# Kernel optimization log

Measured on AMD Instinct MI355X. Metric: run time of the kernel, lower is better.

Reference implementation:

```python
import jax, jax.numpy as jnp
import numpy as np

NUM_AGENTS = 256
STATE_DIM = 12 * NUM_AGENTS
CONTROL_DIM = 4 * NUM_AGENTS
MASS = 0.5
HIDDEN = 100
BATCH = 8192


def lambertw(x):
    # Principal branch for x >= 0 via Halley iterations (jit/vjp friendly).
    w = jnp.log1p(x)
    for _ in range(30):
        ew = jnp.exp(w)
        f = w * ew - x
        denom = ew * (w + 1.0) - (w + 2.0) * f / (2.0 * (w + 1.0))
        w = w - f / denom
    return w


def setup_inputs() -> dict:
    key = jax.random.key(0)
    ks = jax.random.split(key, 8)
    scale1 = 1.0 / np.sqrt(STATE_DIM + 1)
    scale2 = 1.0 / np.sqrt(HIDDEN)
    return {
        "z": jax.random.normal(ks[0], (BATCH, STATE_DIM), dtype=jnp.float32),
        "t": jax.random.uniform(ks[1], (BATCH, 1), dtype=jnp.float32),
        "W1": jax.random.normal(ks[2], (STATE_DIM + 1, HIDDEN), dtype=jnp.float32) * scale1,
        "b1": jnp.zeros((HIDDEN,), dtype=jnp.float32),
        "W2": jax.random.normal(ks[3], (HIDDEN, HIDDEN), dtype=jnp.float32) * scale2,
        "b2": jnp.zeros((HIDDEN,), dtype=jnp.float32),
        "W3": jax.random.normal(ks[4], (HIDDEN, STATE_DIM), dtype=jnp.float32) * scale2,
        "b3": jnp.zeros((STATE_DIM,), dtype=jnp.float32),
    }


def reference(z, t, W1, b1, W2, b2, W3, b3):
    # p_net: MLP on (t, z) producing cost parameters p (B, STATE_DIM)
    x = jnp.concatenate([t, z], axis=-1)
    h = jnp.tanh(x @ W1 + b1)
    h = jnp.tanh(h @ W2 + b2)
    p = h @ W3 + b3

    B = p.shape[0]
    pr = p.reshape(B, NUM_AGENTS, 12)
    # Linear cost vector c over controls: agent components (x,y,z adjoints)/m, psi, theta, phi.
    c = jnp.stack(
        [(pr[..., 6] + pr[..., 7] + pr[..., 8]) / MASS, pr[..., 9], pr[..., 10], pr[..., 11]],
        axis=-1,
    ).reshape(B, CONTROL_DIM)

    # Closed-form solution of min_u c^T u + exp(alpha * ||u||^2), alpha = 0.5/N:
    # u* = -k c with 2*alpha*k*exp(alpha*k^2*s) = 1, s = ||c||^2
    # => k = sqrt(W(s/(2*alpha)) / (2*alpha*s))
    alpha = 0.5 / NUM_AGENTS
    s = jnp.sum(c * c, axis=-1)  # (B,)
    w = lambertw(s / (2.0 * alpha))
    safe_s = jnp.where(s > 0, s, 1.0)
    k = jnp.sqrt(w / (2.0 * alpha * safe_s))
    k = jnp.where(s > 0, k, 0.0)
    ustar = -k[:, None] * c  # (B, CONTROL_DIM)
    return ustar
```

## Files before the change

### kernel.cpp

```cpp
#include <hip/hip_runtime.h>

#define DEV __device__ __forceinline__

typedef __bf16 bf16x8 __attribute__((ext_vector_type(8)));
typedef float f32x4 __attribute__((ext_vector_type(4)));
typedef short s16x8 __attribute__((ext_vector_type(8)));
typedef unsigned short u16x8 __attribute__((ext_vector_type(8)));

constexpr int B_ = 8192;
constexpr int S_ = 3072;
constexpr int H_ = 100;
constexpr int NP_ = 128;
constexpr int C_ = 1024;
constexpr int KS_ = 64;
constexpr int NSPLIT_ = 4;
constexpr int KSP_ = S_ / NSPLIT_;
constexpr int NIT_ = KSP_ / KS_;

constexpr size_t OFF_W1b = 0;
constexpr size_t OFF_W2b = OFF_W1b + (size_t)NP_ * S_ * 2;
constexpr size_t OFF_W3c = OFF_W2b + (size_t)NP_ * NP_ * 2;
constexpr size_t OFF_b3c = OFF_W3c + (size_t)C_ * NP_ * 2;
constexpr size_t OFF_part = OFF_b3c + (size_t)C_ * 4;

DEV unsigned short f2bf(float f) {
  union { float f; unsigned u; } x; x.f = f;
  return (unsigned short)((x.u + 0x7FFFu + ((x.u >> 16) & 1u)) >> 16);
}

DEV float lambertw0(float x) {
  float w = log1pf(x);
#pragma unroll
  for (int i = 0; i < 10; ++i) {
    float ew = expf(w);
    float f = fmaf(w, ew, -x);
    float wp1 = w + 1.0f;
    float den = ew * wp1 - (w + 2.0f) * f / (2.0f * wp1);
    w = w - f / den;
  }
  return w;
}

DEV void gload16(const void* g, void* l) {
  __builtin_amdgcn_global_load_lds((const __attribute__((address_space(1))) unsigned int*)g,
                                   (__attribute__((address_space(3))) unsigned int*)l, 16, 0, 0);
}

__global__ void k0_prep(const float* __restrict__ W1, const float* __restrict__ W2,
                        const float* __restrict__ W3, const float* __restrict__ b3,
                        unsigned char* __restrict__ ws) {
  int idx = blockIdx.x * 256 + threadIdx.x;
  constexpr int R1 = NP_ * S_;
  constexpr int R2 = R1 + NP_ * NP_;
  constexpr int R3 = R2 + C_ * NP_;
  constexpr int R4 = R3 + C_;
  if (idx < R1) {
    int n = idx / S_, k = idx - n * S_;
    float v = (n < H_) ? W1[(size_t)(k + 1) * H_ + n] : 0.0f;
    ((unsigned short*)(ws + OFF_W1b))[idx] = f2bf(v);
  } else if (idx < R2) {
    int j = idx - R1;
    int n = j >> 7, k = j & 127;
    float v = (n < H_ && k < H_) ? W2[(size_t)k * H_ + n] : 0.0f;
    ((unsigned short*)(ws + OFF_W2b))[j] = f2bf(v);
  } else if (idx < R3) {
    int j = idx - R2;
    int n = j >> 7, k = j & 127;
    float v = 0.0f;
    if (k < H_) {
      int a = n >> 2, cmp = n & 3;
      const float* row = W3 + (size_t)k * S_ + a * 12;
      v = (cmp == 0) ? 2.0f * (row[6] + row[7] + row[8]) : row[8 + cmp];
    }
    ((unsigned short*)(ws + OFF_W3c))[j] = f2bf(v);
  } else if (idx < R4) {
    int n = idx - R3;
    int a = n >> 2, cmp = n & 3;
    const float* row = b3 + a * 12;
    float v = (cmp == 0) ? 2.0f * (row[6] + row[7] + row[8]) : row[8 + cmp];
    ((float*)(ws + OFF_b3c))[n] = v;
  }
}

__global__ __launch_bounds__(256, 4) void k1_gemm1(
    const float* __restrict__ z, const unsigned char* __restrict__ wsr,
    float* __restrict__ part) {
  __shared__ __align__(16) unsigned char lds[40 * 1024];
  unsigned char* ldsA = lds;
  unsigned char* ldsB = lds + 8192;

  const int tid = threadIdx.x;
  const int lane = tid & 63;
  const int w = tid >> 6;
  const int m = w & 1;
  const int q = w >> 1;
  const int bid = blockIdx.x;
  const int rt = bid >> 2;
  const int h = bid & 3;
  const int rowbase = rt * 32;
  const int k0 = h * KSP_;

  const unsigned short* W1b = (const unsigned short*)(wsr + OFF_W1b);

  const int zrow = tid >> 3;
  const int zk8 = (tid & 7) * 8;
  const float* zp = z + (size_t)(rowbase + zrow) * S_ + k0 + zk8;
  const int aswz = ((zrow & 7) << 4);
  const int abyte = zrow * 128 + zk8 * 2;

  const int w4 = w * 4;
  const unsigned short* bsrc = W1b + (size_t)(w4 * 8 + (lane >> 3)) * S_ + k0
                               + (((lane & 7) ^ (lane >> 3)) * 8);

  const int r0 = m * 16 + (lane & 15);
  const int kb0 = (lane >> 4) * 16;

  f32x4 acc[4];
#pragma unroll
  for (int e = 0; e < 4; ++e) acc[e] = f32x4{0.f, 0.f, 0.f, 0.f};

#define GLOAD_B(bufoff, kof) do {                                            \
    _Pragma("unroll")                                                        \
    for (int s = 0; s < 4; ++s)                                              \
      gload16(bsrc + (size_t)s * 8 * S_ + (kof),                             \
              ldsB + (bufoff) + (w4 + s) * 1024);                            \
  } while (0)

#define STAGE_A(dst, ZA, ZB) do {                                            \
    u16x8 av;                                                                \
    av[0] = f2bf((ZA).x); av[1] = f2bf((ZA).y);                              \
    av[2] = f2bf((ZA).z); av[3] = f2bf((ZA).w);                              \
    av[4] = f2bf((ZB).x); av[5] = f2bf((ZB).y);                              \
    av[6] = f2bf((ZB).z); av[7] = f2bf((ZB).w);                              \
    *(u16x8*)((dst) + (abyte ^ aswz)) = av;                                  \
  } while (0)

#define COMPUTE(Ac, Bc) do {                                                 \
    bf16x8 a0 = *(const bf16x8*)((Ac) + ((r0 * 128 + 0 + kb0) ^ ((r0 & 7) << 4)));   \
    bf16x8 a1 = *(const bf16x8*)((Ac) + ((r0 * 128 + 64 + kb0) ^ ((r0 & 7) << 4)));  \
    _Pragma("unroll")                                                        \
    for (int e = 0; e < 4; ++e) {                                            \
      int n = q * 64 + e * 16 + (lane & 15);                                 \
      bf16x8 bb0 = *(const bf16x8*)((Bc) + ((n * 128 + 0 + kb0) ^ ((n & 7) << 4)));  \
      bf16x8 bb1 = *(const bf16x8*)((Bc) + ((n * 128 + 64 + kb0) ^ ((n & 7) << 4))); \
      acc[e] = __builtin_amdgcn_mfma_f32_16x16x32_bf16(a0, bb0, acc[e], 0, 0, 0);    \
      acc[e] = __builtin_amdgcn_mfma_f32_16x16x32_bf16(a1, bb1, acc[e], 0, 0, 0);    \
    }                                                                        \
  } while (0)

  GLOAD_B(0, 0);
  {
    float4 za = *(const float4*)(zp);
    float4 zb = *(const float4*)(zp + 4);
    STAGE_A(ldsA, za, zb);
  }
  __syncthreads();

  for (int it = 0; it < NIT_; ++it) {
    const int cur = it & 1;
    const bool more = (it + 1 < NIT_);
    float4 za, zb;
    if (more) {
      GLOAD_B((cur ^ 1) * 16384, (size_t)(it + 1) * KS_);
      za = *(const float4*)(zp + (it + 1) * KS_);
      zb = *(const float4*)(zp + (it + 1) * KS_ + 4);
    }
    COMPUTE(ldsA + cur * 4096, ldsB + cur * 16384);
    if (more) STAGE_A(ldsA + (cur ^ 1) * 4096, za, zb);
    __syncthreads();
  }
#undef GLOAD_B
#undef STAGE_A
#undef COMPUTE

  float* pout = part + (size_t)h * B_ * NP_;
#pragma unroll
  for (int e = 0; e < 4; ++e) {
    int col = q * 64 + e * 16 + (lane & 15);
#pragma unroll
    for (int i = 0; i < 4; ++i) {
      int r = m * 16 + ((lane >> 4) << 2) + i;
      pout[(size_t)(rowbase + r) * NP_ + col] = acc[e][i];
    }
  }
}

__global__ __launch_bounds__(512, 2) void k2_fused(
    const float* __restrict__ part, const float* __restrict__ t,
    const float* __restrict__ W1, const float* __restrict__ b1,
    const float* __restrict__ b2, const unsigned char* __restrict__ wsr,
    float* __restrict__ uo) {
  __shared__ __align__(16) unsigned char ldsA[8192];
  __shared__ __align__(16) unsigned char ldsB[2][32768];
  __shared__ float s_part[32][4];
  __shared__ float k_lds[32];

  const int tid = threadIdx.x;
  const int lane = tid & 63;
  const int w = tid >> 6;
  const int m = w & 1;
  const int q = w >> 1;
  const int rowbase = blockIdx.x * 32;

  const unsigned short* W2b = (const unsigned short*)(wsr + OFF_W2b);
  const unsigned short* W3cb = (const unsigned short*)(wsr + OFF_W3c);
  const float* b3c = (const float*)(wsr + OFF_b3c);

  {
    const int row = tid >> 4;
    const int col0 = (tid & 15) * 8;
    const float* p0 = part + (size_t)(rowbase + row) * NP_ + col0;
    f32x4 v[2];
#pragma unroll
    for (int p = 0; p < 2; ++p) {
      v[p] = *(const f32x4*)(p0 + p * 4);
#pragma unroll
      for (int hh = 1; hh < NSPLIT_; ++hh) {
        f32x4 u2 = *(const f32x4*)(p0 + (size_t)hh * B_ * NP_ + p * 4);
        v[p][0] += u2[0]; v[p][1] += u2[1]; v[p][2] += u2[2]; v[p][3] += u2[3];
      }
    }
    const float tv = t[rowbase + row];
    u16x8 o;
#pragma unroll
    for (int j = 0; j < 8; ++j) {
      int col = col0 + j;
      float b1c = (col < H_) ? b1[col] : 0.0f;
      float w1t = (col < H_) ? W1[col] : 0.0f;
      float pre = v[j >> 2][j & 3] + b1c + tv * w1t;
      o[j] = f2bf(tanhf(pre));
    }
    *(u16x8*)(ldsA + ((row * 256 + col0 * 2) ^ ((row & 7) << 4))) = o;
  }
#pragma unroll
  for (int s = 0; s < 4; ++s) {
    int p = s * 512 + tid;
    int n = p >> 4, k16 = p & 15;
    s16x8 v2 = *(const s16x8*)(W2b + n * 128 + k16 * 8);
    *(s16x8*)(ldsB[1] + ((n * 256 + k16 * 16) ^ ((n & 7) << 4))) = v2;
    s16x8 v3 = *(const s16x8*)(W3cb + (size_t)n * NP_ + k16 * 8);
    *(s16x8*)(ldsB[0] + ((n * 256 + k16 * 16) ^ ((n & 7) << 4))) = v3;
  }
  if (tid < 128) s_part[tid >> 2][tid & 3] = 0.0f;
  __syncthreads();

  const int r0 = m * 16 + (lane & 15);
  const int kb0 = (lane >> 4) * 16;

  f32x4 acc2[2];
  acc2[0] = f32x4{0.f, 0.f, 0.f, 0.f};
  acc2[1] = f32x4{0.f, 0.f, 0.f, 0.f};
#pragma unroll
  for (int ks = 0; ks < 4; ++ks) {
    bf16x8 a = *(const bf16x8*)(ldsA + ((r0 * 256 + ks * 64 + kb0) ^ ((r0 & 7) << 4)));
#pragma unroll
    for (int e = 0; e < 2; ++e) {
      int n = (q * 2 + e) * 16 + (lane & 15);
      bf16x8 b = *(const bf16x8*)(ldsB[1] + ((n * 256 + ks * 64 + kb0) ^ ((n & 7) << 4)));
      acc2[e] = __builtin_amdgcn_mfma_f32_16x16x32_bf16(a, b, acc2[e], 0, 0, 0);
    }
  }
  __syncthreads();
#pragma unroll
  for (int e = 0; e < 2; ++e) {
    int col = (q * 2 + e) * 16 + (lane & 15);
    float b2c = (col < H_) ? b2[col] : 0.0f;
#pragma unroll
    for (int i = 0; i < 4; ++i) {
      int r = m * 16 + ((lane >> 4) << 2) + i;
      float hh = tanhf(acc2[e][i] + b2c);
      *(unsigned short*)(ldsA + ((r * 256 + col * 2) ^ ((r & 7) << 4))) = f2bf(hh);
    }
  }
  __syncthreads();

  bf16x8 af[4];
#pragma unroll
  for (int ks = 0; ks < 4; ++ks)
    af[ks] = *(const bf16x8*)(ldsA + ((r0 * 256 + ks * 64 + kb0) ^ ((r0 & 7) << 4)));

  f32x4 fr[16];
#pragma unroll
  for (int i = 0; i < 16; ++i) fr[i] = f32x4{0.f, 0.f, 0.f, 0.f};

#pragma unroll 8
  for (int ch = 0; ch < 8; ++ch) {
    const int cur = ch & 1;
    const bool more = ch < 7;
    s16x8 st0, st1, st2, st3;
    if (more) {
      int base = (ch + 1) * 128;
      { int p = tid;            int n = p >> 4, k16 = p & 15; st0 = *(const s16x8*)(W3cb + (size_t)(base + n) * NP_ + k16 * 8); }
      { int p = 512 + tid;      int n = p >> 4, k16 = p & 15; st1 = *(const s16x8*)(W3cb + (size_t)(base + n) * NP_ + k16 * 8); }
      { int p = 1024 + tid;     int n = p >> 4, k16 = p & 15; st2 = *(const s16x8*)(W3cb + (size_t)(base + n) * NP_ + k16 * 8); }
      { int p = 1536 + tid;     int n = p >> 4, k16 = p & 15; st3 = *(const s16x8*)(W3cb + (size_t)(base + n) * NP_ + k16 * 8); }
    }
#pragma unroll
    for (int e = 0; e < 2; ++e) {
      int nloc = (q + 4 * e) * 16 + (lane & 15);
#pragma unroll
      for (int ks = 0; ks < 4; ++ks) {
        bf16x8 b = *(const bf16x8*)(ldsB[cur] + ((nloc * 256 + ks * 64 + kb0) ^ ((nloc & 7) << 4)));
        fr[ch * 2 + e] = __builtin_amdgcn_mfma_f32_16x16x32_bf16(af[ks], b, fr[ch * 2 + e], 0, 0, 0);
      }
    }
    if (more) {
      unsigned char* Bn = ldsB[cur ^ 1];
      { int p = tid;        int n = p >> 4, k16 = p & 15; *(s16x8*)(Bn + ((n * 256 + k16 * 16) ^ ((n & 7) << 4))) = st0; }
      { int p = 512 + tid;  int n = p >> 4, k16 = p & 15; *(s16x8*)(Bn + ((n * 256 + k16 * 16) ^ ((n & 7) << 4))) = st1; }
      { int p = 1024 + tid; int n = p >> 4, k16 = p & 15; *(s16x8*)(Bn + ((n * 256 + k16 * 16) ^ ((n & 7) << 4))) = st2; }
      { int p = 1536 + tid; int n = p >> 4, k16 = p & 15; *(s16x8*)(Bn + ((n * 256 + k16 * 16) ^ ((n & 7) << 4))) = st3; }
    }
    __syncthreads();
  }

#pragma unroll
  for (int fi = 0; fi < 16; ++fi) {
    int ch = fi >> 1, e = fi & 1;
    int col = (ch * 8 + q + 4 * e) * 16 + (lane & 15);
    float bc = b3c[col];
    fr[fi][0] += bc; fr[fi][1] += bc; fr[fi][2] += bc; fr[fi][3] += bc;
  }
#pragma unroll
  for (int i = 0; i < 4; ++i) {
    float v = 0.f;
#pragma unroll
    for (int fi = 0; fi < 16; ++fi) v += fr[fi][i] * fr[fi][i];
    v += __shfl_xor(v, 1);
    v += __shfl_xor(v, 2);
    v += __shfl_xor(v, 4);
    v += __shfl_xor(v, 8);
    if ((lane & 15) == 0) s_part[m * 16 + ((lane >> 4) << 2) + i][q] = v;
  }
  __syncthreads();
  if (tid < 32) {
    float s = s_part[tid][0] + s_part[tid][1] + s_part[tid][2] + s_part[tid][3];
    float kk = 0.0f;
    if (s > 0.0f) {
      float wv = lambertw0(s * 256.0f);
      kk = sqrtf(wv * 256.0f / s);
    }
    k_lds[tid] = kk;
  }
  __syncthreads();
#pragma unroll
  for (int fi = 0; fi < 16; ++fi) {
    int ch = fi >> 1, e = fi & 1;
    int col = (ch * 8 + q + 4 * e) * 16 + (lane & 15);
#pragma unroll
    for (int i = 0; i < 4; ++i) {
      int r = m * 16 + ((lane >> 4) << 2) + i;
      uo[(size_t)(rowbase + r) * C_ + col] = -k_lds[r] * fr[fi][i];
    }
  }
}

extern "C" void kernel_launch(void* const* d_in, const int* in_sizes, int n_in,
                              void* d_out, int out_size, void* d_ws, size_t ws_size,
                              hipStream_t stream) {
  const float* z  = (const float*)d_in[0];
  const float* t  = (const float*)d_in[1];
  const float* W1 = (const float*)d_in[2];
  const float* b1 = (const float*)d_in[3];
  const float* W2 = (const float*)d_in[4];
  const float* b2 = (const float*)d_in[5];
  const float* W3 = (const float*)d_in[6];
  const float* b3 = (const float*)d_in[7];
  float* out = (float*)d_out;
  unsigned char* ws = (unsigned char*)d_ws;
  float* part = (float*)(ws + OFF_part);

  constexpr int PREP_ELEMS = NP_ * S_ + NP_ * NP_ + C_ * NP_ + C_;
  k0_prep<<<(PREP_ELEMS + 255) / 256, 256, 0, stream>>>(W1, W2, W3, b3, ws);
  k1_gemm1<<<B_ / 32 * NSPLIT_, 256, 0, stream>>>(z, ws, part);
  k2_fused<<<B_ / 32, 512, 0, stream>>>(part, t, W1, b1, b2, ws, out);
}
```

Before: 51.53 us.

## Load z fragments directly into registers with 64-row tiles and 8-way split-K

The first GEMM no longer stages z through LDS. Each wave now loads its own 16 rows of z straight into registers, converts them to bf16 and feeds them as MFMA A operands, and computes all 128 output columns. The row tile grows from 32 to 64, which halves how often the bf16 W1 tile is reloaded, and split-K goes from 4 to 8 to keep enough blocks in flight. The trade-offs are less coalesced per-lane z loads and twice as many partial sums to write and reduce downstream.

```diff
diff --git a/kernel.cpp b/kernel.cpp
--- a/kernel.cpp
+++ b/kernel.cpp
@@ -13,9 +13,10 @@
 constexpr int NP_ = 128;
 constexpr int C_ = 1024;
 constexpr int KS_ = 64;
-constexpr int NSPLIT_ = 4;
+constexpr int NSPLIT_ = 8;
 constexpr int KSP_ = S_ / NSPLIT_;
 constexpr int NIT_ = KSP_ / KS_;
+constexpr int MT_ = 64;
 
 constexpr size_t OFF_W1b = 0;
 constexpr size_t OFF_W2b = OFF_W1b + (size_t)NP_ * S_ * 2;
@@ -85,101 +86,105 @@
 __global__ __launch_bounds__(256, 4) void k1_gemm1(
     const float* __restrict__ z, const unsigned char* __restrict__ wsr,
     float* __restrict__ part) {
-  __shared__ __align__(16) unsigned char lds[40 * 1024];
-  unsigned char* ldsA = lds;
-  unsigned char* ldsB = lds + 8192;
+  __shared__ __align__(16) unsigned char ldsB[2][16384];
 
   const int tid = threadIdx.x;
   const int lane = tid & 63;
   const int w = tid >> 6;
-  const int m = w & 1;
-  const int q = w >> 1;
   const int bid = blockIdx.x;
-  const int rt = bid >> 2;
-  const int h = bid & 3;
-  const int rowbase = rt * 32;
+  const int rt = bid >> 3;
+  const int h = bid & 7;
+  const int rowbase = rt * MT_;
   const int k0 = h * KSP_;
 
   const unsigned short* W1b = (const unsigned short*)(wsr + OFF_W1b);
 
-  const int zrow = tid >> 3;
-  const int zk8 = (tid & 7) * 8;
-  const float* zp = z + (size_t)(rowbase + zrow) * S_ + k0 + zk8;
-  const int aswz = ((zrow & 7) << 4);
-  const int abyte = zrow * 128 + zk8 * 2;
+  const int arow = rowbase + w * 16 + (lane & 15);
+  const int o8 = (lane >> 4) * 8;
+  const float* zrp = z + (size_t)arow * S_ + k0 + o8;
 
   const int w4 = w * 4;
   const unsigned short* bsrc = W1b + (size_t)(w4 * 8 + (lane >> 3)) * S_ + k0
                                + (((lane & 7) ^ (lane >> 3)) * 8);
 
-  const int r0 = m * 16 + (lane & 15);
   const int kb0 = (lane >> 4) * 16;
 
-  f32x4 acc[4];
-#pragma unroll
-  for (int e = 0; e < 4; ++e) acc[e] = f32x4{0.f, 0.f, 0.f, 0.f};
-
-#define GLOAD_B(bufoff, kof) do {                                            \
+  f32x4 acc[8];
+#pragma unroll
+  for (int e = 0; e < 8; ++e) acc[e] = f32x4{0.f, 0.f, 0.f, 0.f};
+
+#define GLOAD_B(buf, kof) do {                                               \
     _Pragma("unroll")                                                        \
     for (int s = 0; s < 4; ++s)                                              \
       gload16(bsrc + (size_t)s * 8 * S_ + (kof),                             \
-              ldsB + (bufoff) + (w4 + s) * 1024);                            \
+              ldsB[buf] + (w4 + s) * 1024);                                  \
   } while (0)
 
-#define STAGE_A(dst, ZA, ZB) do {                                            \
-    u16x8 av;                                                                \
-    av[0] = f2bf((ZA).x); av[1] = f2bf((ZA).y);                              \
-    av[2] = f2bf((ZA).z); av[3] = f2bf((ZA).w);                              \
-    av[4] = f2bf((ZB).x); av[5] = f2bf((ZB).y);                              \
-    av[6] = f2bf((ZB).z); av[7] = f2bf((ZB).w);                              \
-    *(u16x8*)((dst) + (abyte ^ aswz)) = av;                                  \
+#define ISSUE_A(F0A, F0B, F1A, F1B, kof) do {                                \
+    (F0A) = *(const float4*)(zrp + (kof));                                   \
+    (F0B) = *(const float4*)(zrp + (kof) + 4);                               \
+    (F1A) = *(const float4*)(zrp + (kof) + 32);                              \
+    (F1B) = *(const float4*)(zrp + (kof) + 36);                              \
   } while (0)
 
-#define COMPUTE(Ac, Bc) do {                                                 \
-    bf16x8 a0 = *(const bf16x8*)((Ac) + ((r0 * 128 + 0 + kb0) ^ ((r0 & 7) << 4)));   \
-    bf16x8 a1 = *(const bf16x8*)((Ac) + ((r0 * 128 + 64 + kb0) ^ ((r0 & 7) << 4)));  \
+#define COMPUTE(F0A, F0B, F1A, F1B, buf) do {                                \
+    union { u16x8 u; bf16x8 b; } a0c, a1c;                                   \
+    a0c.u[0] = f2bf((F0A).x); a0c.u[1] = f2bf((F0A).y);                      \
+    a0c.u[2] = f2bf((F0A).z); a0c.u[3] = f2bf((F0A).w);                      \
+    a0c.u[4] = f2bf((F0B).x); a0c.u[5] = f2bf((F0B).y);                      \
+    a0c.u[6] = f2bf((F0B).z); a0c.u[7] = f2bf((F0B).w);                      \
+    a1c.u[0] = f2bf((F1A).x); a1c.u[1] = f2bf((F1A).y);                      \
+    a1c.u[2] = f2bf((F1A).z); a1c.u[3] = f2bf((F1A).w);                      \
+    a1c.u[4] = f2bf((F1B).x); a1c.u[5] = f2bf((F1B).y);                      \
+    a1c.u[6] = f2bf((F1B).z); a1c.u[7] = f2bf((F1B).w);                      \
     _Pragma("unroll")                                                        \
-    for (int e = 0; e < 4; ++e) {                                            \
-      int n = q * 64 + e * 16 + (lane & 15);                                 \
-      bf16x8 bb0 = *(const bf16x8*)((Bc) + ((n * 128 + 0 + kb0) ^ ((n & 7) << 4)));  \
-      bf16x8 bb1 = *(const bf16x8*)((Bc) + ((n * 128 + 64 + kb0) ^ ((n & 7) << 4))); \
-      acc[e] = __builtin_amdgcn_mfma_f32_16x16x32_bf16(a0, bb0, acc[e], 0, 0, 0);    \
-      acc[e] = __builtin_amdgcn_mfma_f32_16x16x32_bf16(a1, bb1, acc[e], 0, 0, 0);    \
+    for (int e = 0; e < 8; ++e) {                                            \
+      int n = e * 16 + (lane & 15);                                          \
+      bf16x8 bb0 = *(const bf16x8*)(ldsB[buf] + ((n * 128 + 0 + kb0) ^ ((n & 7) << 4)));  \
+      bf16x8 bb1 = *(const bf16x8*)(ldsB[buf] + ((n * 128 + 64 + kb0) ^ ((n & 7) << 4))); \
+      acc[e] = __builtin_amdgcn_mfma_f32_16x16x32_bf16(a0c.b, bb0, acc[e], 0, 0, 0);      \
+      acc[e] = __builtin_amdgcn_mfma_f32_16x16x32_bf16(a1c.b, bb1, acc[e], 0, 0, 0);      \
     }                                                                        \
   } while (0)
 
+  float4 e0a, e0b, e1a, e1b;
+  float4 o0a, o0b, o1a, o1b;
+
   GLOAD_B(0, 0);
-  {
-    float4 za = *(const float4*)(zp);
-    float4 zb = *(const float4*)(zp + 4);
-    STAGE_A(ldsA, za, zb);
-  }
-  __syncthreads();
-
-  for (int it = 0; it < NIT_; ++it) {
-    const int cur = it & 1;
-    const bool more = (it + 1 < NIT_);
-    float4 za, zb;
-    if (more) {
-      GLOAD_B((cur ^ 1) * 16384, (size_t)(it + 1) * KS_);
-      za = *(const float4*)(zp + (it + 1) * KS_);
-      zb = *(const float4*)(zp + (it + 1) * KS_ + 4);
-    }
-    COMPUTE(ldsA + cur * 4096, ldsB + cur * 16384);
-    if (more) STAGE_A(ldsA + (cur ^ 1) * 4096, za, zb);
-    __syncthreads();
+  ISSUE_A(e0a, e0b, e1a, e1b, 0);
+  __syncthreads();
+
+  for (int tt = 0; tt < NIT_; tt += 2) {
+    {
+      const bool more = (tt + 1 < NIT_);
+      if (more) {
+        GLOAD_B(1, (size_t)(tt + 1) * KS_);
+        ISSUE_A(o0a, o0b, o1a, o1b, (tt + 1) * KS_);
+      }
+      COMPUTE(e0a, e0b, e1a, e1b, 0);
+      __syncthreads();
+    }
+    {
+      const bool more = (tt + 2 < NIT_);
+      if (more) {
+        GLOAD_B(0, (size_t)(tt + 2) * KS_);
+        ISSUE_A(e0a, e0b, e1a, e1b, (tt + 2) * KS_);
+      }
+      COMPUTE(o0a, o0b, o1a, o1b, 1);
+      __syncthreads();
+    }
   }
 #undef GLOAD_B
-#undef STAGE_A
+#undef ISSUE_A
 #undef COMPUTE
 
   float* pout = part + (size_t)h * B_ * NP_;
 #pragma unroll
-  for (int e = 0; e < 4; ++e) {
-    int col = q * 64 + e * 16 + (lane & 15);
+  for (int e = 0; e < 8; ++e) {
+    int col = e * 16 + (lane & 15);
 #pragma unroll
     for (int i = 0; i < 4; ++i) {
-      int r = m * 16 + ((lane >> 4) << 2) + i;
+      int r = w * 16 + ((lane >> 4) << 2) + i;
       pout[(size_t)(rowbase + r) * NP_ + col] = acc[e][i];
     }
   }
@@ -372,6 +377,6 @@
 
   constexpr int PREP_ELEMS = NP_ * S_ + NP_ * NP_ + C_ * NP_ + C_;
   k0_prep<<<(PREP_ELEMS + 255) / 256, 256, 0, stream>>>(W1, W2, W3, b3, ws);
-  k1_gemm1<<<B_ / 32 * NSPLIT_, 256, 0, stream>>>(z, ws, part);
+  k1_gemm1<<<(B_ / MT_) * NSPLIT_, 256, 0, stream>>>(z, ws, part);
   k2_fused<<<B_ / 32, 512, 0, stream>>>(part, t, W1, b1, b2, ws, out);
 }
```

New measurement: 56.66 us. +10.0%, slower.
